# Kernel optimization log

Measured on AMD Instinct MI355X. Metric: run time of the kernel, lower is better.

Reference implementation:

```python
import jax, jax.numpy as jnp
import numpy as np

E, T, IN, OUT = 8, 16384, 1024, 1024  # n_groups, total_tokens, in_features, out_features


def setup_inputs() -> dict:
    key = jax.random.key(0)
    kx, kw, ks = jax.random.split(key, 3)
    x = jax.random.normal(kx, (T, IN), dtype=jnp.float32)
    # kaiming_uniform-ish scale for weight [E, OUT, IN]
    weight = jax.random.normal(kw, (E, OUT, IN), dtype=jnp.float32) * (1.0 / np.sqrt(IN))
    # ragged segment lengths that sum exactly to T (random cut points)
    cuts = jnp.sort(jax.random.randint(ks, (E - 1,), 0, T + 1)).astype(jnp.int32)
    seg_lens = jnp.diff(
        jnp.concatenate([jnp.zeros((1,), jnp.int32), cuts, jnp.full((1,), T, jnp.int32)])
    )
    return {"x": x, "weight": weight, "seg_lens": seg_lens}


def reference(x, weight, seg_lens):
    # Grouped GEMM: row t of x is multiplied by weight[g(t)].T where g(t) is the
    # segment (expert) that token t falls into per seg_lens. trans_b=True.
    n_groups = weight.shape[0]
    bounds = jnp.cumsum(seg_lens)                                  # [E]
    seg_id = jnp.searchsorted(bounds, jnp.arange(x.shape[0]), side="right")  # [T]
    y = jnp.zeros((x.shape[0], weight.shape[1]), dtype=x.dtype)
    for e in range(n_groups):  # small fixed loop over groups
        y = y + jnp.where((seg_id == e)[:, None], x @ weight[e].T, 0)
    return y
```

## Files before the change

kernel.cpp:

```cpp
#include <hip/hip_runtime.h>

#define T_TOK  16384
#define IN_F   1024
#define OUT_F  1024
#define NE     8

typedef __bf16 bf16;
typedef bf16  bf16x4 __attribute__((ext_vector_type(4)));
typedef bf16  bf16x8 __attribute__((ext_vector_type(8)));
typedef float f32x4  __attribute__((ext_vector_type(4)));

#define CVT_THREADS 256
#define NX_CHUNKS (T_TOK * IN_F / 4)
#define NW_CHUNKS (NE * OUT_F * IN_F / 4)
#define NO_CHUNKS (T_TOK * OUT_F / 4)
#define NCVT_CHUNKS (NX_CHUNKS + NW_CHUNKS)
#define NALL_CHUNKS (NCVT_CHUNKS + NO_CHUNKS)

__global__ __launch_bounds__(CVT_THREADS)
void cvt_and_zero(const float* __restrict__ x, const float* __restrict__ w,
                  bf16* __restrict__ xb, bf16* __restrict__ wb,
                  float* __restrict__ out)
{
    for (int i = blockIdx.x * CVT_THREADS + threadIdx.x; i < NALL_CHUNKS;
         i += gridDim.x * CVT_THREADS) {
        if (i < NCVT_CHUNKS) {
            const bool isx = (i < NX_CHUNKS);
            const int  j   = isx ? i : i - NX_CHUNKS;
            f32x4 v = isx ? ((const f32x4*)x)[j] : ((const f32x4*)w)[j];
            bf16x4 h;
            #pragma unroll
            for (int k = 0; k < 4; ++k) h[k] = (bf16)v[k];
            if (isx) ((bf16x4*)xb)[j] = h;
            else     ((bf16x4*)wb)[j] = h;
        } else {
            f32x4 z = {0.f, 0.f, 0.f, 0.f};
            ((f32x4*)out)[i - NCVT_CHUNKS] = z;
        }
    }
}

#define BM 256
#define BN 256
#define BK 64
#define GTHREADS 512
#define NBLOCKS 256
#define KCH (IN_F / BK)

__device__ __forceinline__ void gld_lds16(const bf16* g, bf16* l) {
    __builtin_amdgcn_global_load_lds(
        (const __attribute__((address_space(1))) void*)g,
        (__attribute__((address_space(3))) void*)l,
        16, 0, 0);
}

__global__ __launch_bounds__(GTHREADS)
void grouped_gemm_streamk(const bf16* __restrict__ xb,
                          const bf16* __restrict__ wb,
                          const int*  __restrict__ seg_lens,
                          float* __restrict__ out)
{
    __shared__ __align__(16) bf16 As[2][BM * BK];
    __shared__ __align__(16) bf16 Bs[2][BN * BK];

    const int tid  = threadIdx.x;
    const int lane = tid & 63;
    const int wave = tid >> 6;
    const int wr   = wave >> 2;
    const int wc   = wave & 3;
    const int quad = lane >> 4;
    const int l16  = lane & 15;
    const int rq   = lane >> 3;
    const int ke   = (lane & 7) * 8;
    const int q0   = wave * 4;

    int sl[NE];
    #pragma unroll
    for (int e = 0; e < NE; ++e) sl[e] = seg_lens[e];

    int n_slots = 0;
    #pragma unroll
    for (int e = 0; e < NE; ++e) n_slots += (sl[e] + BM - 1) >> 8;

    const int L    = n_slots * (OUT_F / BN);
    const int U    = L * KCH;
    const int base = U >> 8;
    const int rem  = U & 255;
    const int b    = blockIdx.x;
    int u          = b * base + (b < rem ? b : rem);
    const int uend = u + base + (b < rem ? 1 : 0);

    while (u < uend) {
        const int tile = u >> 4;
        const int kc0  = u & (KCH - 1);
        int kc1 = kc0 + (uend - u);
        if (kc1 > KCH) kc1 = KCH;
        u += kc1 - kc0;

        const int slot = tile >> 2;
        const int col0 = (tile & 3) << 8;

        int e_sel = -1, row0 = 0, rows = 0;
        {
            int start = 0, acct = 0;
            #pragma unroll
            for (int e = 0; e < NE; ++e) {
                int len = sl[e];
                int nt  = (len + BM - 1) >> 8;
                if (e_sel < 0 && slot >= acct && slot < acct + nt) {
                    e_sel = e;
                    row0  = start + (slot - acct) * BM;
                    int rm = start + len - row0;
                    rows = rm < BM ? rm : BM;
                }
                acct  += nt;
                start += len;
            }
        }

        const bf16* wbase = wb + ((size_t)e_sel * OUT_F + (size_t)col0) * IN_F;

        const bf16* ga[4];
        const bf16* gb[4];
        #pragma unroll
        for (int i = 0; i < 4; ++i) {
            int q  = wave * 4 + i;
            int ra = row0 + q * 8 + rq;
            if (ra > T_TOK - 1) ra = T_TOK - 1;
            ga[i] = xb + (size_t)ra * IN_F + ke;
            gb[i] = wbase + (size_t)(q * 8 + rq) * IN_F + ke;
        }

        f32x4 acc[8][4] = {};

        {
            const int kb = kc0 * BK;
            #pragma unroll
            for (int i = 0; i < 4; ++i) {
                gld_lds16(ga[i] + kb, &As[0][(q0 + i) * 512]);
                gld_lds16(gb[i] + kb, &Bs[0][(q0 + i) * 512]);
            }
        }
        __syncthreads();

        int cur = 0;
        for (int ks = kc0; ks < kc1; ++ks) {
            const int kn = (ks + 1) * BK;
            if (ks + 1 < kc1) {
                #pragma unroll
                for (int i = 0; i < 4; ++i) {
                    gld_lds16(ga[i] + kn, &As[cur ^ 1][(q0 + i) * 512]);
                    gld_lds16(gb[i] + kn, &Bs[cur ^ 1][(q0 + i) * 512]);
                }
            }

            #pragma unroll
            for (int kk = 0; kk < 2; ++kk) {
                bf16x8 af[8], bfr[4];
                #pragma unroll
                for (int t = 0; t < 8; ++t)
                    af[t] = *(const bf16x8*)(
                        &As[cur][(wr * 128 + t * 16 + l16) * BK + kk * 32 + quad * 8]);
                #pragma unroll
                for (int v = 0; v < 4; ++v)
                    bfr[v] = *(const bf16x8*)(
                        &Bs[cur][(wc * 64 + v * 16 + l16) * BK + kk * 32 + quad * 8]);
                #pragma unroll
                for (int t = 0; t < 8; ++t)
                    #pragma unroll
                    for (int v = 0; v < 4; ++v)
                        acc[t][v] = __builtin_amdgcn_mfma_f32_16x16x32_bf16(
                            af[t], bfr[v], acc[t][v], 0, 0, 0);
            }

            __syncthreads();
            cur ^= 1;
        }

        if (kc0 == 0 && kc1 == KCH) {
            #pragma unroll
            for (int t = 0; t < 8; ++t) {
                #pragma unroll
                for (int r = 0; r < 4; ++r) {
                    int row = wr * 128 + t * 16 + quad * 4 + r;
                    if (row < rows) {
                        size_t ob = (size_t)(row0 + row) * OUT_F + col0 + wc * 64;
                        #pragma unroll
                        for (int v = 0; v < 4; ++v)
                            out[ob + v * 16 + l16] = acc[t][v][r];
                    }
                }
            }
        } else {
            #pragma unroll
            for (int t = 0; t < 8; ++t) {
                #pragma unroll
                for (int r = 0; r < 4; ++r) {
                    int row = wr * 128 + t * 16 + quad * 4 + r;
                    if (row < rows) {
                        size_t ob = (size_t)(row0 + row) * OUT_F + col0 + wc * 64;
                        #pragma unroll
                        for (int v = 0; v < 4; ++v)
                            unsafeAtomicAdd(&out[ob + v * 16 + l16], acc[t][v][r]);
                    }
                }
            }
        }
    }
}

#define FBM 128
#define FBK 32
#define FTHREADS 256
#define FROW_SLOTS 136

__global__ __launch_bounds__(FTHREADS)
void grouped_gemm_f32io_bf16(const float* __restrict__ x,
                             const float* __restrict__ wgt,
                             const int*  __restrict__ seg_lens,
                             float* __restrict__ out)
{
    __shared__ __align__(16) bf16 Asf[FBM * FBK];
    __shared__ __align__(16) bf16 Bsf[FBM * FBK];

    const int m    = blockIdx.y;
    const int col0 = blockIdx.x * FBM;

    int e_sel = -1, row0 = 0, rows = 0;
    {
        int start = 0, acct = 0;
        #pragma unroll
        for (int e = 0; e < NE; ++e) {
            int len = seg_lens[e];
            int nt  = (len + FBM - 1) >> 7;
            if (e_sel < 0 && m >= acct && m < acct + nt) {
                e_sel = e;
                row0  = start + (m - acct) * FBM;
                int rem = start + len - row0;
                rows = rem < FBM ? rem : FBM;
            }
            acct  += nt;
            start += len;
        }
    }
    if (e_sel < 0) return;

    const int tid  = threadIdx.x;
    const int lane = tid & 63;
    const int wave = tid >> 6;
    const int wm   = (wave >> 1) * 64;
    const int wn   = (wave & 1) * 64;
    const int quad = lane >> 4;
    const int l16  = lane & 15;

    const float* wbase = wgt + ((size_t)e_sel * OUT_F + (size_t)col0) * IN_F;

    f32x4 acc[4][4] = {};

    for (int k0 = 0; k0 < IN_F; k0 += FBK) {
        f32x4 a_st[4], b_st[4];
        #pragma unroll
        for (int t = 0; t < 4; ++t) {
            int c  = t * FTHREADS + tid;
            int rg = row0 + (c >> 3);
            if (rg > T_TOK - 1) rg = T_TOK - 1;
            a_st[t] = *(const f32x4*)(x + (size_t)rg * IN_F + k0 + (c & 7) * 4);
            b_st[t] = *(const f32x4*)(wbase + (size_t)(c >> 3) * IN_F + k0 + (c & 7) * 4);
        }

        __syncthreads();

        #pragma unroll
        for (int t = 0; t < 4; ++t) {
            int c = t * FTHREADS + tid;
            bf16x4 ha, hb;
            #pragma unroll
            for (int j = 0; j < 4; ++j) { ha[j] = (bf16)a_st[t][j]; hb[j] = (bf16)b_st[t][j]; }
            *(bf16x4*)(&Asf[(c >> 3) * FBK + (c & 7) * 4]) = ha;
            *(bf16x4*)(&Bsf[(c >> 3) * FBK + (c & 7) * 4]) = hb;
        }
        __syncthreads();

        bf16x8 af[4], bfr[4];
        #pragma unroll
        for (int t = 0; t < 4; ++t)
            af[t] = *(const bf16x8*)(&Asf[(wm + t * 16 + l16) * FBK + quad * 8]);
        #pragma unroll
        for (int v = 0; v < 4; ++v)
            bfr[v] = *(const bf16x8*)(&Bsf[(wn + v * 16 + l16) * FBK + quad * 8]);

        #pragma unroll
        for (int t = 0; t < 4; ++t)
            #pragma unroll
            for (int v = 0; v < 4; ++v)
                acc[t][v] = __builtin_amdgcn_mfma_f32_16x16x32_bf16(
                    af[t], bfr[v], acc[t][v], 0, 0, 0);
    }

    #pragma unroll
    for (int t = 0; t < 4; ++t) {
        #pragma unroll
        for (int r = 0; r < 4; ++r) {
            int row = wm + t * 16 + quad * 4 + r;
            if (row < rows) {
                size_t ob = (size_t)(row0 + row) * OUT_F + col0;
                #pragma unroll
                for (int v = 0; v < 4; ++v)
                    out[ob + wn + v * 16 + l16] = acc[t][v][r];
            }
        }
    }
}

extern "C" void kernel_launch(void* const* d_in, const int* in_sizes, int n_in,
                              void* d_out, int out_size, void* d_ws, size_t ws_size,
                              hipStream_t stream) {
    const float* x   = (const float*)d_in[0];
    const float* wgt = (const float*)d_in[1];
    const int*   seg = (const int*)d_in[2];
    float* out = (float*)d_out;

    const size_t xbytes = (size_t)T_TOK * IN_F * sizeof(bf16);
    const size_t wbytes = (size_t)NE * OUT_F * IN_F * sizeof(bf16);

    if (ws_size >= xbytes + wbytes) {
        bf16* xb = (bf16*)d_ws;
        bf16* wb = (bf16*)((char*)d_ws + xbytes);
        cvt_and_zero<<<dim3(2048, 1, 1), dim3(CVT_THREADS, 1, 1), 0, stream>>>(
            x, wgt, xb, wb, out);
        grouped_gemm_streamk<<<dim3(NBLOCKS, 1, 1), dim3(GTHREADS, 1, 1), 0, stream>>>(
            xb, wb, seg, out);
    } else {
        grouped_gemm_f32io_bf16<<<dim3(OUT_F / FBM, FROW_SLOTS, 1),
                                  dim3(FTHREADS, 1, 1), 0, stream>>>(x, wgt, seg, out);
    }
}
```

Baseline: 235.4 us.

## Use hybrid data-parallel first wave plus stream-K tail for grouped GEMM

Replaces pure stream-K scheduling with a hybrid. Each of the 256 blocks first computes one full output tile over the whole K range and writes it with plain stores. Only the remaining tiles are split stream-K style across blocks, using atomic adds. This is meant to cut atomic traffic and partial-tile overhead for most tiles. The tail still has split-K atomics, and if the tile count is only slightly above 256 the tail may be poorly balanced.

```diff
diff --git a/kernel.cpp b/kernel.cpp
--- a/kernel.cpp
+++ b/kernel.cpp
@@ -54,11 +54,31 @@
         16, 0, 0);
 }
 
+__device__ __forceinline__ void resolve_slot(const int* sl, int slot,
+                                             int& e_sel, int& row0, int& rows)
+{
+    e_sel = -1; row0 = 0; rows = 0;
+    int start = 0, acct = 0;
+    #pragma unroll
+    for (int e = 0; e < NE; ++e) {
+        int len = sl[e];
+        int nt  = (len + BM - 1) >> 8;
+        if (e_sel < 0 && slot >= acct && slot < acct + nt) {
+            e_sel = e;
+            row0  = start + (slot - acct) * BM;
+            int rm = start + len - row0;
+            rows = rm < BM ? rm : BM;
+        }
+        acct  += nt;
+        start += len;
+    }
+}
+
 __global__ __launch_bounds__(GTHREADS)
-void grouped_gemm_streamk(const bf16* __restrict__ xb,
-                          const bf16* __restrict__ wb,
-                          const int*  __restrict__ seg_lens,
-                          float* __restrict__ out)
+void grouped_gemm_hybrid(const bf16* __restrict__ xb,
+                         const bf16* __restrict__ wb,
+                         const int*  __restrict__ seg_lens,
+                         float* __restrict__ out)
 {
     __shared__ __align__(16) bf16 As[2][BM * BK];
     __shared__ __align__(16) bf16 Bs[2][BN * BK];
@@ -73,6 +93,7 @@
     const int rq   = lane >> 3;
     const int ke   = (lane & 7) * 8;
     const int q0   = wave * 4;
+    const int b    = blockIdx.x;
 
     int sl[NE];
     #pragma unroll
@@ -81,42 +102,13 @@
     int n_slots = 0;
     #pragma unroll
     for (int e = 0; e < NE; ++e) n_slots += (sl[e] + BM - 1) >> 8;
-
-    const int L    = n_slots * (OUT_F / BN);
-    const int U    = L * KCH;
-    const int base = U >> 8;
-    const int rem  = U & 255;
-    const int b    = blockIdx.x;
-    int u          = b * base + (b < rem ? b : rem);
-    const int uend = u + base + (b < rem ? 1 : 0);
-
-    while (u < uend) {
-        const int tile = u >> 4;
-        const int kc0  = u & (KCH - 1);
-        int kc1 = kc0 + (uend - u);
-        if (kc1 > KCH) kc1 = KCH;
-        u += kc1 - kc0;
-
-        const int slot = tile >> 2;
-        const int col0 = (tile & 3) << 8;
-
-        int e_sel = -1, row0 = 0, rows = 0;
-        {
-            int start = 0, acct = 0;
-            #pragma unroll
-            for (int e = 0; e < NE; ++e) {
-                int len = sl[e];
-                int nt  = (len + BM - 1) >> 8;
-                if (e_sel < 0 && slot >= acct && slot < acct + nt) {
-                    e_sel = e;
-                    row0  = start + (slot - acct) * BM;
-                    int rm = start + len - row0;
-                    rows = rm < BM ? rm : BM;
-                }
-                acct  += nt;
-                start += len;
-            }
-        }
+    const int L = n_slots * (OUT_F / BN);
+
+    if (b < L) {
+        const int slot = b >> 2;
+        const int col0 = (b & 3) << 8;
+        int e_sel, row0, rows;
+        resolve_slot(sl, slot, e_sel, row0, rows);
 
         const bf16* wbase = wb + ((size_t)e_sel * OUT_F + (size_t)col0) * IN_F;
 
@@ -133,20 +125,18 @@
 
         f32x4 acc[8][4] = {};
 
-        {
-            const int kb = kc0 * BK;
-            #pragma unroll
-            for (int i = 0; i < 4; ++i) {
-                gld_lds16(ga[i] + kb, &As[0][(q0 + i) * 512]);
-                gld_lds16(gb[i] + kb, &Bs[0][(q0 + i) * 512]);
-            }
+        #pragma unroll
+        for (int i = 0; i < 4; ++i) {
+            gld_lds16(ga[i], &As[0][(q0 + i) * 512]);
+            gld_lds16(gb[i], &Bs[0][(q0 + i) * 512]);
         }
         __syncthreads();
 
         int cur = 0;
-        for (int ks = kc0; ks < kc1; ++ks) {
+        #pragma unroll
+        for (int ks = 0; ks < KCH; ++ks) {
             const int kn = (ks + 1) * BK;
-            if (ks + 1 < kc1) {
+            if (ks + 1 < KCH) {
                 #pragma unroll
                 for (int i = 0; i < 4; ++i) {
                     gld_lds16(ga[i] + kn, &As[cur ^ 1][(q0 + i) * 512]);
@@ -177,21 +167,100 @@
             cur ^= 1;
         }
 
-        if (kc0 == 0 && kc1 == KCH) {
-            #pragma unroll
-            for (int t = 0; t < 8; ++t) {
-                #pragma unroll
-                for (int r = 0; r < 4; ++r) {
-                    int row = wr * 128 + t * 16 + quad * 4 + r;
-                    if (row < rows) {
-                        size_t ob = (size_t)(row0 + row) * OUT_F + col0 + wc * 64;
+        #pragma unroll
+        for (int t = 0; t < 8; ++t) {
+            #pragma unroll
+            for (int r = 0; r < 4; ++r) {
+                int row = wr * 128 + t * 16 + quad * 4 + r;
+                if (row < rows) {
+                    size_t ob = (size_t)(row0 + row) * OUT_F + col0 + wc * 64;
+                    #pragma unroll
+                    for (int v = 0; v < 4; ++v)
+                        out[ob + v * 16 + l16] = acc[t][v][r];
+                }
+            }
+        }
+    }
+
+    const int Uleft = (L - NBLOCKS) * KCH;
+    if (Uleft <= 0) return;
+    {
+        const int base = Uleft >> 8;
+        const int rem  = Uleft & 255;
+        int u    = NBLOCKS * KCH + b * base + (b < rem ? b : rem);
+        int uend = u + base + (b < rem ? 1 : 0);
+
+        while (u < uend) {
+            const int tile = u >> 4;
+            const int kc0  = u & (KCH - 1);
+            int kc1 = kc0 + (uend - u);
+            if (kc1 > KCH) kc1 = KCH;
+            u += kc1 - kc0;
+
+            const int slot = tile >> 2;
+            const int col0 = (tile & 3) << 8;
+            int e_sel, row0, rows;
+            resolve_slot(sl, slot, e_sel, row0, rows);
+
+            const bf16* wbase = wb + ((size_t)e_sel * OUT_F + (size_t)col0) * IN_F;
+
+            const bf16* ga[4];
+            const bf16* gb[4];
+            #pragma unroll
+            for (int i = 0; i < 4; ++i) {
+                int q  = wave * 4 + i;
+                int ra = row0 + q * 8 + rq;
+                if (ra > T_TOK - 1) ra = T_TOK - 1;
+                ga[i] = xb + (size_t)ra * IN_F + ke;
+                gb[i] = wbase + (size_t)(q * 8 + rq) * IN_F + ke;
+            }
+
+            f32x4 acc[8][4] = {};
+
+            {
+                const int kb = kc0 * BK;
+                #pragma unroll
+                for (int i = 0; i < 4; ++i) {
+                    gld_lds16(ga[i] + kb, &As[0][(q0 + i) * 512]);
+                    gld_lds16(gb[i] + kb, &Bs[0][(q0 + i) * 512]);
+                }
+            }
+            __syncthreads();
+
+            int cur = 0;
+            for (int ks = kc0; ks < kc1; ++ks) {
+                const int kn = (ks + 1) * BK;
+                if (ks + 1 < kc1) {
+                    #pragma unroll
+                    for (int i = 0; i < 4; ++i) {
+                        gld_lds16(ga[i] + kn, &As[cur ^ 1][(q0 + i) * 512]);
+                        gld_lds16(gb[i] + kn, &Bs[cur ^ 1][(q0 + i) * 512]);
+                    }
+                }
+
+                #pragma unroll
+                for (int kk = 0; kk < 2; ++kk) {
+                    bf16x8 af[8], bfr[4];
+                    #pragma unroll
+                    for (int t = 0; t < 8; ++t)
+                        af[t] = *(const bf16x8*)(
+                            &As[cur][(wr * 128 + t * 16 + l16) * BK + kk * 32 + quad * 8]);
+                    #pragma unroll
+                    for (int v = 0; v < 4; ++v)
+                        bfr[v] = *(const bf16x8*)(
+                            &Bs[cur][(wc * 64 + v * 16 + l16) * BK + kk * 32 + quad * 8]);
+                    #pragma unroll
+                    for (int t = 0; t < 8; ++t)
                         #pragma unroll
                         for (int v = 0; v < 4; ++v)
-                            out[ob + v * 16 + l16] = acc[t][v][r];
-                    }
-                }
-            }
-        } else {
+                            acc[t][v] = __builtin_amdgcn_mfma_f32_16x16x32_bf16(
+                                af[t], bfr[v], acc[t][v], 0, 0, 0);
+                }
+
+                __syncthreads();
+                cur ^= 1;
+            }
+
             #pragma unroll
             for (int t = 0; t < 8; ++t) {
                 #pragma unroll
@@ -328,7 +397,7 @@
         bf16* wb = (bf16*)((char*)d_ws + xbytes);
         cvt_and_zero<<<dim3(2048, 1, 1), dim3(CVT_THREADS, 1, 1), 0, stream>>>(
             x, wgt, xb, wb, out);
-        grouped_gemm_streamk<<<dim3(NBLOCKS, 1, 1), dim3(GTHREADS, 1, 1), 0, stream>>>(
+        grouped_gemm_hybrid<<<dim3(NBLOCKS, 1, 1), dim3(GTHREADS, 1, 1), 0, stream>>>(
             xb, wb, seg, out);
     } else {
         grouped_gemm_f32io_bf16<<<dim3(OUT_F / FBM, FROW_SLOTS, 1),
```

New measurement: 224.8 us. 1.05x faster.
